# Optimization experiments

Hardware: AMD Instinct MI355X
Metric: run time of the kernel (lower is better)

## Reference

```python
import jax, jax.numpy as jnp
import numpy as np

TEMPERATURE = 0.1
NORM_EPS = 1e-12          # F.normalize default eps
SMALL_VAL = float(np.finfo(np.float32).tiny)  # pytorch-metric-learning small_val(float32)
NEG_INF = float(np.finfo(np.float32).min)     # c_f.neg_inf for masked logsumexp


def setup_inputs() -> dict:
    key = jax.random.key(0)
    k1, k2 = jax.random.split(key)
    N, D = 8192, 128
    emb = jax.random.normal(k1, (N, D), dtype=jnp.float32)
    labels = jax.random.randint(k2, (N,), 0, 1000, dtype=jnp.int64)
    return {"emb": emb, "labels": labels}


def reference(emb, labels):
    N = emb.shape[0]
    # F.normalize(emb, dim=1): x / max(||x||, eps)
    norms = jnp.linalg.norm(emb, axis=1, keepdims=True)
    x = emb / jnp.maximum(norms, NORM_EPS)

    # cosine similarity matrix [N, N], scaled by temperature
    mat = jnp.matmul(x, x.T) / TEMPERATURE

    same = labels[:, None] == labels[None, :]
    diag = jnp.eye(N, dtype=bool)
    pos_mask = same & ~diag          # same label, i != j
    keep_mask = ~diag                # pos + neg (all off-diagonal)

    # numerical stability: subtract detached row max (over full row, incl. diagonal)
    mat_max = jax.lax.stop_gradient(jnp.max(mat, axis=1, keepdims=True))
    mat = mat - mat_max

    # masked logsumexp over off-diagonal entries
    masked = jnp.where(keep_mask, mat, NEG_INF)
    denom = jax.nn.logsumexp(masked, axis=1, keepdims=True)  # [N, 1]

    log_prob = mat - denom
    pos_f = pos_mask.astype(mat.dtype)
    mean_log_prob_pos = jnp.sum(pos_f * log_prob, axis=1) / (
        jnp.sum(pos_f, axis=1) + SMALL_VAL
    )
    losses = -mean_log_prob_pos  # per-element losses
    # SumReducer: sum over elements
    return jnp.sum(losses)
```

## Files before the change

### kernel.cpp

```cpp
#include <hip/hip_runtime.h>
#include <hip/hip_bf16.h>


typedef __bf16 bf16_t;
typedef __bf16 bf16x2 __attribute__((ext_vector_type(2)));
typedef __bf16 bf16x8 __attribute__((ext_vector_type(8)));
typedef float f32x16 __attribute__((ext_vector_type(16)));

#define NN 8192
#define DIM 128
#define MAIN_BLOCKS 2080
#define SMALL_VAL 1.17549435e-38f
#define L2E10 14.4269504089f
#define LN2 0.69314718056f

__device__ inline size_t swz(int row, int lane) {
    int f = lane >> 3, hh = (lane >> 2) & 1, j = (lane & 3) << 1;
    return ((size_t)(row >> 5) * 4096) + f * 512 + hh * 256 + (row & 31) * 8 + j;
}

__global__ __launch_bounds__(256) void norm_csum(const float* __restrict__ emb,
                                                 const int* __restrict__ labels,
                                                 bf16_t* __restrict__ xsw,
                                                 float* __restrict__ cd_arr,
                                                 float* __restrict__ sd_arr,
                                                 float* __restrict__ cm1_arr,
                                                 float* __restrict__ se_acc,
                                                 float* __restrict__ out) {
    __shared__ float cs[DIM];
    __shared__ int rowlist[96];
    __shared__ int nrows;
    int cls = blockIdx.x;
    int wv = threadIdx.x >> 6, lane = threadIdx.x & 63;
    if (threadIdx.x < DIM) cs[threadIdx.x] = 0.f;
    if (threadIdx.x == 0) nrows = 0;
    if (threadIdx.x < 8) se_acc[cls * 8 + threadIdx.x] = 0.f;
    if (cls == 0 && threadIdx.x == 0) *out = 0.f;
    __syncthreads();

    float s0 = 0.f, s1 = 0.f;
    const int4* lab4 = (const int4*)(labels + wv * 2048);
#pragma unroll
    for (int it = 0; it < 8; ++it) {
        int4 l = lab4[it * 64 + lane];
        int base = wv * 2048 + it * 256;
#pragma unroll
        for (int cmp = 0; cmp < 4; ++cmp) {
            int li = (cmp == 0) ? l.x : (cmp == 1) ? l.y : (cmp == 2) ? l.z : l.w;
            unsigned long long m = __ballot(li == cls);
            while (m) {
                int bb = __builtin_ctzll(m);
                m &= m - 1;
                int row = base + 4 * bb + cmp;
                float2 v = ((const float2*)emb)[row * 64 + lane];
                float ss = fmaf(v.x, v.x, v.y * v.y);
#pragma unroll
                for (int mm = 1; mm < 64; mm <<= 1) ss += __shfl_xor(ss, mm, 64);
                float inv = 1.0f / fmaxf(sqrtf(ss), 1e-12f);
                bf16x2 o; o.x = (bf16_t)(v.x * inv); o.y = (bf16_t)(v.y * inv);
                *(bf16x2*)(xsw + swz(row, lane)) = o;
                s0 += (float)o.x; s1 += (float)o.y;
                if (lane == 0) {
                    int idx = atomicAdd(&nrows, 1);
                    if (idx < 96) rowlist[idx] = row;
                }
            }
        }
    }
    atomicAdd(&cs[2 * lane], s0);
    atomicAdd(&cs[2 * lane + 1], s1);
    __syncthreads();
    int n = nrows;
    for (int k = wv; k < n; k += 4) {
        int row = rowlist[k];
        bf16x2 xv = *(const bf16x2*)(xsw + swz(row, lane));
        float x0 = (float)xv.x, x1 = (float)xv.y;
        float cdp = fmaf(x0, cs[2 * lane], x1 * cs[2 * lane + 1]);
        float sdp = fmaf(x0, x0, x1 * x1);
#pragma unroll
        for (int mm = 1; mm < 64; mm <<= 1) {
            cdp += __shfl_xor(cdp, mm, 64);
            sdp += __shfl_xor(sdp, mm, 64);
        }
        if (lane == 0) {
            cd_arr[row] = cdp; sd_arr[row] = sdp; cm1_arr[row] = (float)(n - 1);
        }
    }
}

__global__ __launch_bounds__(256, 4) void supcon_main(const bf16_t* __restrict__ xsw,
                                                      float* __restrict__ se_acc) {
    __shared__ bf16_t bst[4 * 4096];
    __shared__ float cols[128];
    if (threadIdx.x < 128) cols[threadIdx.x] = 0.f;

    int b = blockIdx.x;
    int cq = (int)((sqrtf(8.f * (float)b + 1.f) - 1.f) * 0.5f);
    while ((cq + 1) * (cq + 2) / 2 <= b) ++cq;
    while (cq * (cq + 1) / 2 > b) --cq;
    int g = b - cq * (cq + 1) / 2;

    int wv = threadIdx.x >> 6, lane = threadIdx.x & 63;
    int I = 4 * g + wv;
    int c = lane & 31, h = lane >> 5;
    int laneoff = h * 256 + c * 8;

    const bf16_t* abase = xsw + (size_t)I * 4096 + laneoff;
    bf16x8 a[8];
#pragma unroll
    for (int f = 0; f < 8; ++f) a[f] = *(const bf16x8*)(abase + f * 512);

    {
        const uint4* gsrc = (const uint4*)(xsw + (size_t)cq * 4 * 4096);
        uint4* ldst = (uint4*)bst;
#pragma unroll
        for (int i = 0; i < 8; ++i)
            ldst[i * 256 + threadIdx.x] = gsrc[i * 256 + threadIdx.x];
    }
    __syncthreads();

    float se[16];
#pragma unroll
    for (int r = 0; r < 16; ++r) se[r] = 0.f;
    float colacc[4] = {0.f, 0.f, 0.f, 0.f};

#pragma unroll
    for (int t = 0; t < 4; ++t) {
        const bf16_t* bt = bst + t * 4096 + laneoff;
        bf16x8 bfr[8];
#pragma unroll
        for (int f = 0; f < 8; ++f) bfr[f] = *(const bf16x8*)(bt + f * 512);
        f32x16 acc;
#pragma unroll
        for (int r = 0; r < 16; ++r) acc[r] = 0.f;
#pragma unroll
        for (int f = 0; f < 8; ++f)
            acc = __builtin_amdgcn_mfma_f32_32x32x16_bf16(a[f], bfr[f], acc, 0, 0, 0);
        int ct = cq * 4 + t;
        if (ct >= I) {
            float c0 = 0.f, c1 = 0.f, c2 = 0.f, c3 = 0.f;
#pragma unroll
            for (int r = 0; r < 16; ++r) {
                float e = __builtin_amdgcn_exp2f(fmaf(acc[r], L2E10, -L2E10));
                se[r] += e;
                if ((r & 3) == 0) c0 += e; else if ((r & 3) == 1) c1 += e;
                else if ((r & 3) == 2) c2 += e; else c3 += e;
            }
            if (ct > I) colacc[t] = (c0 + c1) + (c2 + c3);
        }
    }

#pragma unroll
    for (int r = 0; r < 16; ++r) {
        float vv = se[r];
#pragma unroll
        for (int m = 1; m < 32; m <<= 1) vv += __shfl_xor(vv, m, 64);
        se[r] = vv;
    }
    if (c == 0) {
        int rowbase = I * 32 + 4 * h;
#pragma unroll
        for (int r = 0; r < 16; ++r)
            atomicAdd(&se_acc[rowbase + (r & 3) + 8 * (r >> 2)], se[r]);
    }

#pragma unroll
    for (int t = 0; t < 4; ++t) {
        float v = colacc[t] + __shfl_xor(colacc[t], 32, 64);
        if (h == 0) atomicAdd(&cols[t * 32 + c], v);
    }
    __syncthreads();
    if (threadIdx.x < 128)
        atomicAdd(&se_acc[cq * 128 + threadIdx.x], cols[threadIdx.x]);
}

__global__ __launch_bounds__(256) void finalize_kernel(const float* __restrict__ se_acc,
                                                       const float* __restrict__ cd_arr,
                                                       const float* __restrict__ sd_arr,
                                                       const float* __restrict__ cm1_arr,
                                                       float* __restrict__ out) {
    __shared__ float part[4];
    int i = blockIdx.x * 256 + threadIdx.x;
    float sd = sd_arr[i], cd = cd_arr[i], cm1 = cm1_arr[i];
    float diag = __builtin_amdgcn_exp2f(fmaf(sd, L2E10, -L2E10));
    float sev  = fmaxf(se_acc[i] - diag, 1e-30f);
    float lse  = fmaf(__builtin_amdgcn_logf(sev), LN2, 10.f);
    float loss = (cm1 * lse - 10.f * (cd - sd)) / (cm1 + SMALL_VAL);
#pragma unroll
    for (int m = 1; m < 64; m <<= 1) loss += __shfl_xor(loss, m, 64);
    int wv = threadIdx.x >> 6;
    if ((threadIdx.x & 63) == 0) part[wv] = loss;
    __syncthreads();
    if (threadIdx.x == 0) atomicAdd(out, part[0] + part[1] + part[2] + part[3]);
}

extern "C" void kernel_launch(void* const* d_in, const int* in_sizes, int n_in,
                              void* d_out, int out_size, void* d_ws, size_t ws_size,
                              hipStream_t stream) {
    const float* emb  = (const float*)d_in[0];
    const int* labels = (const int*)d_in[1];

    char* ws = (char*)d_ws;
    bf16_t* xsw = (bf16_t*)ws;
    float* se   = (float*)(ws + (size_t)NN * DIM * 2);
    float* cd   = se + NN;
    float* sd   = cd + NN;
    float* cm1  = sd + NN;

    norm_csum<<<1024, 256, 0, stream>>>(emb, labels, xsw, cd, sd, cm1, se, (float*)d_out);
    supcon_main<<<MAIN_BLOCKS, 256, 0, stream>>>(xsw, se);
    finalize_kernel<<<NN / 256, 256, 0, stream>>>(se, cd, sd, cm1, (float*)d_out);
}
```

Before: 98.61 us.

## Fuse finalize into main kernel via last-block counter and use DPP reductions

```diff
diff --git a/kernel.cpp b/kernel.cpp
--- a/kernel.cpp
+++ b/kernel.cpp
@@ -17,6 +17,22 @@
 __device__ inline size_t swz(int row, int lane) {
     int f = lane >> 3, hh = (lane >> 2) & 1, j = (lane & 3) << 1;
     return ((size_t)(row >> 5) * 4096) + f * 512 + hh * 256 + (row & 31) * 8 + j;
+}
+
+#define DPPADD(v, ctrl, rmask)                                                         \
+    do {                                                                               \
+        int _t = __builtin_amdgcn_update_dpp(0, __float_as_int((v)), (ctrl), (rmask),  \
+                                             0xf, true);                               \
+        (v) += __int_as_float(_t);                                                     \
+    } while (0)
+
+__device__ inline float half32_sum(float v) {
+    DPPADD(v, 0x111, 0xf);
+    DPPADD(v, 0x112, 0xf);
+    DPPADD(v, 0x114, 0xf);
+    DPPADD(v, 0x118, 0xf);
+    DPPADD(v, 0x142, 0xa);
+    return v;
 }
 
 __global__ __launch_bounds__(256) void norm_csum(const float* __restrict__ emb,
@@ -26,7 +42,7 @@
                                                  float* __restrict__ sd_arr,
                                                  float* __restrict__ cm1_arr,
                                                  float* __restrict__ se_acc,
-                                                 float* __restrict__ out) {
+                                                 int* __restrict__ done_cnt) {
     __shared__ float cs[DIM];
     __shared__ int rowlist[96];
     __shared__ int nrows;
@@ -35,7 +51,7 @@
     if (threadIdx.x < DIM) cs[threadIdx.x] = 0.f;
     if (threadIdx.x == 0) nrows = 0;
     if (threadIdx.x < 8) se_acc[cls * 8 + threadIdx.x] = 0.f;
-    if (cls == 0 && threadIdx.x == 0) *out = 0.f;
+    if (cls == 0 && threadIdx.x == 0) *done_cnt = 0;
     __syncthreads();
 
     float s0 = 0.f, s1 = 0.f;
@@ -89,9 +105,16 @@
 }
 
 __global__ __launch_bounds__(256, 4) void supcon_main(const bf16_t* __restrict__ xsw,
-                                                      float* __restrict__ se_acc) {
+                                                      float* __restrict__ se_acc,
+                                                      const float* __restrict__ cd_arr,
+                                                      const float* __restrict__ sd_arr,
+                                                      const float* __restrict__ cm1_arr,
+                                                      int* __restrict__ done_cnt,
+                                                      float* __restrict__ out) {
     __shared__ bf16_t bst[4 * 4096];
     __shared__ float cols[128];
+    __shared__ int lastflag;
+    __shared__ float part[4];
     if (threadIdx.x < 128) cols[threadIdx.x] = 0.f;
 
     int b = blockIdx.x;
@@ -151,13 +174,8 @@
     }
 
 #pragma unroll
-    for (int r = 0; r < 16; ++r) {
-        float vv = se[r];
-#pragma unroll
-        for (int m = 1; m < 32; m <<= 1) vv += __shfl_xor(vv, m, 64);
-        se[r] = vv;
-    }
-    if (c == 0) {
+    for (int r = 0; r < 16; ++r) se[r] = half32_sum(se[r]);
+    if (c == 31) {
         int rowbase = I * 32 + 4 * h;
 #pragma unroll
         for (int r = 0; r < 16; ++r)
@@ -172,26 +190,32 @@
     __syncthreads();
     if (threadIdx.x < 128)
         atomicAdd(&se_acc[cq * 128 + threadIdx.x], cols[threadIdx.x]);
-}
-
-__global__ __launch_bounds__(256) void finalize_kernel(const float* __restrict__ se_acc,
-                                                       const float* __restrict__ cd_arr,
-                                                       const float* __restrict__ sd_arr,
-                                                       const float* __restrict__ cm1_arr,
-                                                       float* __restrict__ out) {
-    __shared__ float part[4];
-    int i = blockIdx.x * 256 + threadIdx.x;
-    float sd = sd_arr[i], cd = cd_arr[i], cm1 = cm1_arr[i];
-    float diag = __builtin_amdgcn_exp2f(fmaf(sd, L2E10, -L2E10));
-    float sev  = fmaxf(se_acc[i] - diag, 1e-30f);
-    float lse  = fmaf(__builtin_amdgcn_logf(sev), LN2, 10.f);
-    float loss = (cm1 * lse - 10.f * (cd - sd)) / (cm1 + SMALL_VAL);
-#pragma unroll
-    for (int m = 1; m < 64; m <<= 1) loss += __shfl_xor(loss, m, 64);
-    int wv = threadIdx.x >> 6;
-    if ((threadIdx.x & 63) == 0) part[wv] = loss;
-    __syncthreads();
-    if (threadIdx.x == 0) atomicAdd(out, part[0] + part[1] + part[2] + part[3]);
+
+    __threadfence();
+    __syncthreads();
+    if (threadIdx.x == 0) {
+        int prev = atomicAdd(done_cnt, 1);
+        lastflag = (prev == MAIN_BLOCKS - 1) ? 1 : 0;
+    }
+    __syncthreads();
+    if (lastflag == 0) return;
+    __threadfence();
+
+    float total = 0.f;
+#pragma unroll 4
+    for (int k = 0; k < 32; ++k) {
+        int i = (k << 8) + threadIdx.x;
+        float sd = sd_arr[i], cd = cd_arr[i], cm1 = cm1_arr[i];
+        float diag = __builtin_amdgcn_exp2f(fmaf(sd, L2E10, -L2E10));
+        float sev  = fmaxf(se_acc[i] - diag, 1e-30f);
+        float lse  = fmaf(__builtin_amdgcn_logf(sev), LN2, 10.f);
+        total += (cm1 * lse - 10.f * (cd - sd)) / (cm1 + SMALL_VAL);
+    }
+#pragma unroll
+    for (int m = 1; m < 64; m <<= 1) total += __shfl_xor(total, m, 64);
+    if (lane == 0) part[wv] = total;
+    __syncthreads();
+    if (threadIdx.x == 0) *out = part[0] + part[1] + part[2] + part[3];
 }
 
 extern "C" void kernel_launch(void* const* d_in, const int* in_sizes, int n_in,
@@ -206,8 +230,8 @@
     float* cd   = se + NN;
     float* sd   = cd + NN;
     float* cm1  = sd + NN;
-
-    norm_csum<<<1024, 256, 0, stream>>>(emb, labels, xsw, cd, sd, cm1, se, (float*)d_out);
-    supcon_main<<<MAIN_BLOCKS, 256, 0, stream>>>(xsw, se);
-    finalize_kernel<<<NN / 256, 256, 0, stream>>>(se, cd, sd, cm1, (float*)d_out);
-}
+    int* done   = (int*)(cm1 + NN);
+
+    norm_csum<<<1024, 256, 0, stream>>>(emb, labels, xsw, cd, sd, cm1, se, done);
+    supcon_main<<<MAIN_BLOCKS, 256, 0, stream>>>(xsw, se, cd, sd, cm1, done, (float*)d_out);
+}
```

New measurement: 213.9 us. +116.9%, slower.
